# Performance work log

Measured on AMD Instinct MI355X. Metric: run time of the kernel, lower is better.

Reference implementation:

```python
import jax, jax.numpy as jnp
import numpy as np


def setup_inputs() -> dict:
    key = jax.random.key(0)
    k1, k2 = jax.random.split(key)
    img_render_points = jax.random.normal(k1, (128, 128, 2), dtype=jnp.float32)
    ref_catheter_contour_point_cloud = jax.random.normal(k2, (16384, 2), dtype=jnp.float32)
    return {
        "img_render_points": img_render_points,
        "ref_catheter_contour_point_cloud": ref_catheter_contour_point_cloud,
    }


def reference(img_render_points, ref_catheter_contour_point_cloud):
    # Flatten to point cloud (N, 2)
    pc = img_render_points.reshape(-1, 2)
    ref = ref_catheter_contour_point_cloud  # (M, 2)
    # Pairwise Euclidean distances (N, M); torch.norm(..., dim=2) equivalent
    diff = pc[:, None, :] - ref[None, :, :]          # (N, M, 2)
    distances = jnp.sqrt(jnp.sum(diff * diff, axis=-1))  # (N, M)
    min_d1 = jnp.min(distances, axis=1)  # nearest ref point for each render point
    min_d2 = jnp.min(distances, axis=0)  # nearest render point for each ref point
    chamfer_loss = jnp.sum(min_d1) + jnp.sum(min_d2)
    return chamfer_loss
```

## Files before the change

### kernel.cpp

```cpp
#include <hip/hip_runtime.h>
#include <math.h>

#define NPTS  16384
#define BLK   256
#define Q     8
#define QB    (NPTS / (BLK * Q))
#define TCH   128
#define CHUNK (NPTS / TCH)
#define U     (CHUNK / 2)


__global__ __launch_bounds__(BLK, 6) void cc_min_kernel(
        const float2* __restrict__ pc,
        const float2* __restrict__ ref,
        float* __restrict__ ws,
        float* __restrict__ out) {
    __shared__ float4 sxy[U];
    __shared__ float2 sz[U];

    int b   = blockIdx.x;
    int dir = b / (QB * TCH);
    int rem = b % (QB * TCH);
    int qb  = rem / TCH;
    int ch  = rem % TCH;

    if (b == 0 && threadIdx.x == 0) out[0] = 0.0f;

    const float2* __restrict__ qry = dir ? ref : pc;
    const float2* __restrict__ tgt = dir ? pc  : ref;

    if (threadIdx.x < U) {
        int u = threadIdx.x;
        float4 t2 = ((const float4*)tgt)[ch * U + u];
        sxy[u] = make_float4(-2.0f * t2.x, -2.0f * t2.y,
                             -2.0f * t2.z, -2.0f * t2.w);
        sz[u] = make_float2(fmaf(t2.x, t2.x, t2.y * t2.y),
                            fmaf(t2.z, t2.z, t2.w * t2.w));
    }

    float px[Q], py[Q], pn[Q], m[Q];
    int qbase = qb * (BLK * Q) + threadIdx.x;
#pragma unroll
    for (int j = 0; j < Q; ++j) {
        float2 p = qry[qbase + j * BLK];
        px[j] = p.x;
        py[j] = p.y;
        pn[j] = fmaf(p.x, p.x, p.y * p.y);
        m[j]  = INFINITY;
    }
    __syncthreads();

#pragma unroll 8
    for (int u = 0; u < U; ++u) {
        float4 xy = sxy[u];
        float2 z  = sz[u];
#pragma unroll
        for (int j = 0; j < Q; ++j) {
            float s1 = fmaf(px[j], xy.x, fmaf(py[j], xy.y, z.x));
            float s2 = fmaf(px[j], xy.z, fmaf(py[j], xy.w, z.y));
            m[j] = fminf(fminf(m[j], s1), s2);
        }
    }

    float* wrow = ws + (size_t)ch * (2 * NPTS) + dir * NPTS + qbase;
#pragma unroll
    for (int j = 0; j < Q; ++j) {
        wrow[j * BLK] = fmaxf(m[j] + pn[j], 0.0f);
    }
}

__global__ __launch_bounds__(BLK) void cc_final_kernel(
        const float* __restrict__ ws, float* __restrict__ out) {
    int q = blockIdx.x * BLK + threadIdx.x;

    float m0 = INFINITY, m1 = INFINITY, m2 = INFINITY, m3 = INFINITY;
#pragma unroll 8
    for (int ch = 0; ch < TCH; ch += 4) {
        m0 = fminf(m0, ws[(size_t)(ch + 0) * (2 * NPTS) + q]);
        m1 = fminf(m1, ws[(size_t)(ch + 1) * (2 * NPTS) + q]);
        m2 = fminf(m2, ws[(size_t)(ch + 2) * (2 * NPTS) + q]);
        m3 = fminf(m3, ws[(size_t)(ch + 3) * (2 * NPTS) + q]);
    }
    float s = sqrtf(fminf(fminf(m0, m1), fminf(m2, m3)));

#pragma unroll
    for (int off = 32; off > 0; off >>= 1)
        s += __shfl_down(s, off, 64);

    if ((threadIdx.x & 63) == 0)
        atomicAdd(out, s);
}

extern "C" void kernel_launch(void* const* d_in, const int* in_sizes, int n_in,
                              void* d_out, int out_size, void* d_ws, size_t ws_size,
                              hipStream_t stream) {
    const float2* pc  = (const float2*)d_in[0];
    const float2* ref = (const float2*)d_in[1];
    float* out = (float*)d_out;
    float* ws  = (float*)d_ws;

    cc_min_kernel<<<2 * QB * TCH, BLK, 0, stream>>>(pc, ref, ws, out);
    cc_final_kernel<<<(2 * NPTS) / BLK, BLK, 0, stream>>>(ws, out);
}
```

Measured before the change: 99.89 us.

## Halve target chunks, pack four targets per LDS group, widen final reduction

Target chunks per block are halved, so each block scans twice as many targets and the workspace holds half as many partial minima. Targets are packed four at a time into 12-float LDS groups read with three float4 loads, which lowers LDS load instructions per target. The final reduction kernel uses 128-thread blocks and 16 independent loads per thread to expose more memory-level parallelism. The trade-off is half as many min-kernel blocks, which means fewer waves to hide latency, plus a looser occupancy hint.

```diff
diff --git a/kernel.cpp b/kernel.cpp
--- a/kernel.cpp
+++ b/kernel.cpp
@@ -5,18 +5,17 @@
 #define BLK   256
 #define Q     8
 #define QB    (NPTS / (BLK * Q))
-#define TCH   128
+#define TCH   64
 #define CHUNK (NPTS / TCH)
-#define U     (CHUNK / 2)
+#define G     (CHUNK / 4)
 
 
-__global__ __launch_bounds__(BLK, 6) void cc_min_kernel(
+__global__ __launch_bounds__(BLK, 4) void cc_min_kernel(
         const float2* __restrict__ pc,
         const float2* __restrict__ ref,
         float* __restrict__ ws,
         float* __restrict__ out) {
-    __shared__ float4 sxy[U];
-    __shared__ float2 sz[U];
+    __shared__ float s6[G * 12];
 
     int b   = blockIdx.x;
     int dir = b / (QB * TCH);
@@ -29,13 +28,20 @@
     const float2* __restrict__ qry = dir ? ref : pc;
     const float2* __restrict__ tgt = dir ? pc  : ref;
 
-    if (threadIdx.x < U) {
-        int u = threadIdx.x;
-        float4 t2 = ((const float4*)tgt)[ch * U + u];
-        sxy[u] = make_float4(-2.0f * t2.x, -2.0f * t2.y,
-                             -2.0f * t2.z, -2.0f * t2.w);
-        sz[u] = make_float2(fmaf(t2.x, t2.x, t2.y * t2.y),
-                            fmaf(t2.z, t2.z, t2.w * t2.w));
+    if (threadIdx.x < G) {
+        int g = threadIdx.x;
+        const float4* t4 = (const float4*)tgt + (size_t)ch * (CHUNK / 2);
+        float4 p01 = t4[2 * g];
+        float4 p23 = t4[2 * g + 1];
+        float4* dst = (float4*)&s6[12 * g];
+        dst[0] = make_float4(-2.0f * p01.x, -2.0f * p01.y,
+                             -2.0f * p01.z, -2.0f * p01.w);
+        dst[1] = make_float4(-2.0f * p23.x, -2.0f * p23.y,
+                             -2.0f * p23.z, -2.0f * p23.w);
+        dst[2] = make_float4(fmaf(p01.x, p01.x, p01.y * p01.y),
+                             fmaf(p01.z, p01.z, p01.w * p01.w),
+                             fmaf(p23.x, p23.x, p23.y * p23.y),
+                             fmaf(p23.z, p23.z, p23.w * p23.w));
     }
 
     float px[Q], py[Q], pn[Q], m[Q];
@@ -50,15 +56,19 @@
     }
     __syncthreads();
 
-#pragma unroll 8
-    for (int u = 0; u < U; ++u) {
-        float4 xy = sxy[u];
-        float2 z  = sz[u];
+#pragma unroll 4
+    for (int g = 0; g < G; ++g) {
+        float4 A = *(const float4*)&s6[12 * g];
+        float4 B = *(const float4*)&s6[12 * g + 4];
+        float4 C = *(const float4*)&s6[12 * g + 8];
 #pragma unroll
         for (int j = 0; j < Q; ++j) {
-            float s1 = fmaf(px[j], xy.x, fmaf(py[j], xy.y, z.x));
-            float s2 = fmaf(px[j], xy.z, fmaf(py[j], xy.w, z.y));
-            m[j] = fminf(fminf(m[j], s1), s2);
+            float s0 = fmaf(px[j], A.x, fmaf(py[j], A.y, C.x));
+            float s1 = fmaf(px[j], A.z, fmaf(py[j], A.w, C.y));
+            float s2 = fmaf(px[j], B.x, fmaf(py[j], B.y, C.z));
+            float s3 = fmaf(px[j], B.z, fmaf(py[j], B.w, C.w));
+            m[j] = fminf(fminf(m[j], s0), s1);
+            m[j] = fminf(fminf(m[j], s2), s3);
         }
     }
 
@@ -69,19 +79,28 @@
     }
 }
 
-__global__ __launch_bounds__(BLK) void cc_final_kernel(
+#define FBLK 128
+__global__ __launch_bounds__(FBLK) void cc_final_kernel(
         const float* __restrict__ ws, float* __restrict__ out) {
-    int q = blockIdx.x * BLK + threadIdx.x;
+    int q = blockIdx.x * FBLK + threadIdx.x;
 
-    float m0 = INFINITY, m1 = INFINITY, m2 = INFINITY, m3 = INFINITY;
-#pragma unroll 8
-    for (int ch = 0; ch < TCH; ch += 4) {
-        m0 = fminf(m0, ws[(size_t)(ch + 0) * (2 * NPTS) + q]);
-        m1 = fminf(m1, ws[(size_t)(ch + 1) * (2 * NPTS) + q]);
-        m2 = fminf(m2, ws[(size_t)(ch + 2) * (2 * NPTS) + q]);
-        m3 = fminf(m3, ws[(size_t)(ch + 3) * (2 * NPTS) + q]);
+    float mm[16];
+#pragma unroll
+    for (int k = 0; k < 16; ++k)
+        mm[k] = ws[(size_t)k * (2 * NPTS) + q];
+#pragma unroll
+    for (int ch = 16; ch < TCH; ch += 16) {
+#pragma unroll
+        for (int k = 0; k < 16; ++k)
+            mm[k] = fminf(mm[k], ws[(size_t)(ch + k) * (2 * NPTS) + q]);
     }
-    float s = sqrtf(fminf(fminf(m0, m1), fminf(m2, m3)));
+#pragma unroll
+    for (int s2 = 8; s2 > 0; s2 >>= 1)
+#pragma unroll
+        for (int k = 0; k < 8; ++k)
+            if (k < s2) mm[k] = fminf(mm[k], mm[k + s2]);
+
+    float s = sqrtf(mm[0]);
 
 #pragma unroll
     for (int off = 32; off > 0; off >>= 1)
@@ -100,5 +119,5 @@
     float* ws  = (float*)d_ws;
 
     cc_min_kernel<<<2 * QB * TCH, BLK, 0, stream>>>(pc, ref, ws, out);
-    cc_final_kernel<<<(2 * NPTS) / BLK, BLK, 0, stream>>>(ws, out);
+    cc_final_kernel<<<(2 * NPTS) / FBLK, FBLK, 0, stream>>>(ws, out);
 }
```

New measurement: 93.02 us. 1.07x faster.

## Compute pairwise distance terms with f16 MFMA using hi/lo split precision

Applied to the files above, without the earlier changes.

The scalar FMA inner loop is replaced by MFMA 16x16x32 f16 matrix instructions. Coordinates are scaled and split into high and low f16 parts so that -2·p·t + |t|^2 is formed as a dot product on the matrix cores, and the per-query min is reduced with lane shuffles. The chunk count drops from 128 to 16, and the query norm, sqrt and unscale move into the final kernel. Accuracy now depends on the f16 hi/lo decomposition. The column reduction uses cross-lane shuffles and each tile is evaluated twice against tile pairs.

```diff
diff --git a/kernel.cpp b/kernel.cpp
--- a/kernel.cpp
+++ b/kernel.cpp
@@ -1,87 +1,146 @@
 #include <hip/hip_runtime.h>
 #include <math.h>
 
+
 #define NPTS  16384
 #define BLK   256
-#define Q     8
-#define QB    (NPTS / (BLK * Q))
-#define TCH   128
+#define TCH   16
 #define CHUNK (NPTS / TCH)
-#define U     (CHUNK / 2)
+#define TT    (CHUNK / 16)
+#define QPB   512
+#define QBN   (NPTS / QPB)
+#define SCALE 16.0f
+#define INVS  0.0625f
+
+typedef _Float16 f16x8 __attribute__((ext_vector_type(8)));
+typedef float    f32x4 __attribute__((ext_vector_type(4)));
 
 
-__global__ __launch_bounds__(BLK, 6) void cc_min_kernel(
+__global__ __launch_bounds__(BLK, 4) void cc_min_kernel(
         const float2* __restrict__ pc,
         const float2* __restrict__ ref,
         float* __restrict__ ws,
         float* __restrict__ out) {
-    __shared__ float4 sxy[U];
-    __shared__ float2 sz[U];
+    __shared__ f16x8 sB[CHUNK];
 
-    int b   = blockIdx.x;
-    int dir = b / (QB * TCH);
-    int rem = b % (QB * TCH);
-    int qb  = rem / TCH;
-    int ch  = rem % TCH;
+    const int b    = blockIdx.x;
+    const int dir  = b / (QBN * TCH);
+    const int rem  = b % (QBN * TCH);
+    const int qblk = rem / TCH;
+    const int ch   = rem % TCH;
+    const int tid  = threadIdx.x;
+    const int wid  = tid >> 6;
+    const int lane = tid & 63;
 
-    if (b == 0 && threadIdx.x == 0) out[0] = 0.0f;
+    if (b == 0 && tid == 0) out[0] = 0.0f;
 
     const float2* __restrict__ qry = dir ? ref : pc;
     const float2* __restrict__ tgt = dir ? pc  : ref;
 
-    if (threadIdx.x < U) {
-        int u = threadIdx.x;
-        float4 t2 = ((const float4*)tgt)[ch * U + u];
-        sxy[u] = make_float4(-2.0f * t2.x, -2.0f * t2.y,
-                             -2.0f * t2.z, -2.0f * t2.w);
-        sz[u] = make_float2(fmaf(t2.x, t2.x, t2.y * t2.y),
-                            fmaf(t2.z, t2.z, t2.w * t2.w));
+#pragma unroll
+    for (int r = 0; r < CHUNK / BLK; ++r) {
+        int i = r * BLK + tid;
+        float2 t = tgt[ch * CHUNK + i];
+        float xs = t.x * SCALE, ys = t.y * SCALE;
+        _Float16 hx = (_Float16)xs; _Float16 lx = (_Float16)(xs - (float)hx);
+        _Float16 hy = (_Float16)ys; _Float16 ly = (_Float16)(ys - (float)hy);
+        float zz = fmaf(xs, xs, ys * ys);
+        _Float16 hz = (_Float16)zz; _Float16 lz = (_Float16)(zz - (float)hz);
+        f16x8 p;
+        p[0] = (_Float16)(-2.0f * (float)hx);
+        p[1] = (_Float16)(-2.0f * (float)lx);
+        p[2] = p[0];
+        p[3] = (_Float16)(-2.0f * (float)hy);
+        p[4] = (_Float16)(-2.0f * (float)ly);
+        p[5] = p[3];
+        p[6] = hz;
+        p[7] = lz;
+        sB[i] = p;
     }
 
-    float px[Q], py[Q], pn[Q], m[Q];
-    int qbase = qb * (BLK * Q) + threadIdx.x;
+    const int q0 = qblk * QPB + wid * 128;
+    f16x8 A[8];
 #pragma unroll
-    for (int j = 0; j < Q; ++j) {
-        float2 p = qry[qbase + j * BLK];
-        px[j] = p.x;
-        py[j] = p.y;
-        pn[j] = fmaf(p.x, p.x, p.y * p.y);
-        m[j]  = INFINITY;
+    for (int qt = 0; qt < 8; ++qt) {
+        f16x8 a;
+#pragma unroll
+        for (int e = 0; e < 8; ++e) a[e] = (_Float16)0.0f;
+        if (lane < 16) {
+            float2 qp = qry[q0 + qt * 16 + lane];
+            float xs = qp.x * SCALE, ys = qp.y * SCALE;
+            _Float16 hx = (_Float16)xs; _Float16 lx = (_Float16)(xs - (float)hx);
+            _Float16 hy = (_Float16)ys; _Float16 ly = (_Float16)(ys - (float)hy);
+            a[0] = hx; a[1] = hx; a[2] = lx;
+            a[3] = hy; a[4] = hy; a[5] = ly;
+            a[6] = (_Float16)1.0f; a[7] = (_Float16)1.0f;
+        }
+        A[qt] = a;
     }
     __syncthreads();
 
-#pragma unroll 8
-    for (int u = 0; u < U; ++u) {
-        float4 xy = sxy[u];
-        float2 z  = sz[u];
+    f32x4 m[8];
 #pragma unroll
-        for (int j = 0; j < Q; ++j) {
-            float s1 = fmaf(px[j], xy.x, fmaf(py[j], xy.y, z.x));
-            float s2 = fmaf(px[j], xy.z, fmaf(py[j], xy.w, z.y));
-            m[j] = fminf(fminf(m[j], s1), s2);
+    for (int qt = 0; qt < 8; ++qt)
+        m[qt] = (f32x4){INFINITY, INFINITY, INFINITY, INFINITY};
+
+    const f32x4 Z4 = (f32x4){0.f, 0.f, 0.f, 0.f};
+    const int bo = lane & 15;
+    for (int tt = 0; tt < TT; tt += 2) {
+        f16x8 b0 = sB[tt * 16 + bo];
+        f16x8 b1 = sB[tt * 16 + 16 + bo];
+#pragma unroll
+        for (int qt = 0; qt < 8; ++qt) {
+            f32x4 d0 = __builtin_amdgcn_mfma_f32_16x16x32_f16(A[qt], b0, Z4, 0, 0, 0);
+            f32x4 d1 = __builtin_amdgcn_mfma_f32_16x16x32_f16(A[qt], b1, Z4, 0, 0, 0);
+#pragma unroll
+            for (int r = 0; r < 4; ++r)
+                m[qt][r] = fminf(fminf(m[qt][r], d0[r]), d1[r]);
         }
     }
 
-    float* wrow = ws + (size_t)ch * (2 * NPTS) + dir * NPTS + qbase;
 #pragma unroll
-    for (int j = 0; j < Q; ++j) {
-        wrow[j * BLK] = fmaxf(m[j] + pn[j], 0.0f);
+    for (int qt = 0; qt < 8; ++qt) {
+#pragma unroll
+        for (int r = 0; r < 4; ++r) {
+            float v = m[qt][r];
+            v = fminf(v, __shfl_xor(v, 1, 16));
+            v = fminf(v, __shfl_xor(v, 2, 16));
+            v = fminf(v, __shfl_xor(v, 4, 16));
+            v = fminf(v, __shfl_xor(v, 8, 16));
+            m[qt][r] = v;
+        }
+    }
+
+    if ((lane & 15) == 0) {
+        int rowbase = (lane >> 4) * 4;
+        float* prow = ws + (size_t)ch * (2 * NPTS) + dir * NPTS;
+#pragma unroll
+        for (int qt = 0; qt < 8; ++qt) {
+            float4 v = make_float4(m[qt][0], m[qt][1], m[qt][2], m[qt][3]);
+            *(float4*)(prow + q0 + qt * 16 + rowbase) = v;
+        }
     }
 }
 
 __global__ __launch_bounds__(BLK) void cc_final_kernel(
+        const float2* __restrict__ pc, const float2* __restrict__ ref,
         const float* __restrict__ ws, float* __restrict__ out) {
     int q = blockIdx.x * BLK + threadIdx.x;
 
     float m0 = INFINITY, m1 = INFINITY, m2 = INFINITY, m3 = INFINITY;
-#pragma unroll 8
+#pragma unroll
     for (int ch = 0; ch < TCH; ch += 4) {
         m0 = fminf(m0, ws[(size_t)(ch + 0) * (2 * NPTS) + q]);
         m1 = fminf(m1, ws[(size_t)(ch + 1) * (2 * NPTS) + q]);
         m2 = fminf(m2, ws[(size_t)(ch + 2) * (2 * NPTS) + q]);
         m3 = fminf(m3, ws[(size_t)(ch + 3) * (2 * NPTS) + q]);
     }
-    float s = sqrtf(fminf(fminf(m0, m1), fminf(m2, m3)));
+    float msur = fminf(fminf(m0, m1), fminf(m2, m3));
+
+    int dir = q >> 14, qi = q & (NPTS - 1);
+    float2 p = dir ? ref[qi] : pc[qi];
+    float pn = (SCALE * SCALE) * fmaf(p.x, p.x, p.y * p.y);
+    float s = sqrtf(fmaxf(msur + pn, 0.0f)) * INVS;
 
 #pragma unroll
     for (int off = 32; off > 0; off >>= 1)
@@ -99,6 +158,6 @@
     float* out = (float*)d_out;
     float* ws  = (float*)d_ws;
 
-    cc_min_kernel<<<2 * QB * TCH, BLK, 0, stream>>>(pc, ref, ws, out);
-    cc_final_kernel<<<(2 * NPTS) / BLK, BLK, 0, stream>>>(ws, out);
+    cc_min_kernel<<<2 * QBN * TCH, BLK, 0, stream>>>(pc, ref, ws, out);
+    cc_final_kernel<<<(2 * NPTS) / BLK, BLK, 0, stream>>>(pc, ref, ws, out);
 }
```

Result: faster. 87.24 us (-12.7%).
